# Performance work log

Measured on AMD Instinct MI355X. Metric: run time of the kernel, lower is better.

The kernel has to match this reference:

```python
import jax, jax.numpy as jnp
import numpy as np

B, S, D, H = 4, 2048, 1024, 16
HD = D // H  # head dim = 64


def setup_inputs() -> dict:
    key = jax.random.key(0)
    ks = jax.random.split(key, 11)
    s = 1.0 / np.sqrt(D)
    return {
        "xq": jax.random.normal(ks[0], (B, S, D), jnp.float32),
        "xk": jax.random.normal(ks[1], (B, S, D), jnp.float32),
        "xv": jax.random.normal(ks[2], (B, S, D), jnp.float32),
        "wq": jax.random.normal(ks[3], (D, D), jnp.float32) * s,
        "bq": jnp.zeros((D,), jnp.float32),
        "wk": jax.random.normal(ks[4], (D, D), jnp.float32) * s,
        "bk": jnp.zeros((D,), jnp.float32),
        "wv": jax.random.normal(ks[5], (D, D), jnp.float32) * s,
        "bv": jnp.zeros((D,), jnp.float32),
        "wo": jax.random.normal(ks[6], (D, D), jnp.float32) * s,
        "bo": jnp.zeros((D,), jnp.float32),
    }


def reference(xq, xk, xv, wq, bq, wk, bk, wv, bv, wo, bo):
    # linear projections (torch Linear: x @ W.T + b; weights here stored as [in, out])
    q = xq @ wq + bq  # [B,S,D]
    k = xk @ wk + bk
    v = xv @ wv + bv
    # split heads -> [B,H,S,HD]
    q = q.reshape(B, S, H, HD).transpose(0, 2, 1, 3)
    k = k.reshape(B, S, H, HD).transpose(0, 2, 1, 3)
    v = v.reshape(B, S, H, HD).transpose(0, 2, 1, 3)
    # scaled dot-product attention; scale by sqrt(head_dim)
    scores = jnp.einsum('bhqd,bhkd->bhqk', q, k) / jnp.sqrt(jnp.float32(HD))
    attn = jax.nn.softmax(scores, axis=-1)  # [B,H,S,S]
    out = jnp.einsum('bhqk,bhkd->bhqd', attn, v)
    # merge heads -> [B,S,D]
    concat = out.transpose(0, 2, 1, 3).reshape(B, S, D)
    return concat @ wo + bo
```

## Files before the change

kernel.cpp:

```cpp
#include <hip/hip_runtime.h>
#include <hip/hip_bf16.h>

typedef unsigned short u16;
typedef short bf16x8 __attribute__((ext_vector_type(8)));
typedef float f32x4  __attribute__((ext_vector_type(4)));
typedef unsigned short u16x4 __attribute__((ext_vector_type(4)));

#define B_  4
#define S_  2048
#define D_  1024
#define H_  16
#define HD_ 64
#define M_  (B_ * S_)

__device__ __forceinline__ u16 f2bf(float f) {
    unsigned int u = __builtin_bit_cast(unsigned int, f);
    u += 0x7fffu + ((u >> 16) & 1u);
    return (u16)(u >> 16);
}
__device__ __forceinline__ void gload_lds16(const void* g, void* l) {
    __builtin_amdgcn_global_load_lds(
        (const __attribute__((address_space(1))) void*)g,
        (__attribute__((address_space(3))) void*)l, 16, 0, 0);
}
__device__ __forceinline__ unsigned int cvtpk_bf16(float a, float b) {
    unsigned int r;
    asm("v_cvt_pk_bf16_f32 %0, %1, %2" : "=v"(r) : "v"(a), "v"(b));
    return r;
}

__global__ __launch_bounds__(256) void k_transpose_w(
    const float* __restrict__ w0, const float* __restrict__ w1,
    const float* __restrict__ w2, const float* __restrict__ w3,
    u16* __restrict__ wtbase) {
    __shared__ float tile[32][33];
    const float* W = blockIdx.z == 0 ? w0 : blockIdx.z == 1 ? w1
                   : blockIdx.z == 2 ? w2 : w3;
    u16* Wt = wtbase + (size_t)blockIdx.z * (D_ * D_);
    const int tx = threadIdx.x, ty = threadIdx.y;
    const int bx = blockIdx.x * 32, by = blockIdx.y * 32;
#pragma unroll
    for (int i = 0; i < 4; ++i)
        tile[ty + 8 * i][tx] = W[(size_t)(by + ty + 8 * i) * D_ + bx + tx];
    __syncthreads();
#pragma unroll
    for (int i = 0; i < 4; ++i)
        Wt[(size_t)(bx + ty + 8 * i) * D_ + by + tx] = f2bf(tile[tx][ty + 8 * i]);
}

__global__ __launch_bounds__(256) void k_gemm_qkv(
    const float* __restrict__ xq, const float* __restrict__ xk,
    const float* __restrict__ xv, const u16* __restrict__ wtbase,
    const float* __restrict__ bq, const float* __restrict__ bk,
    const float* __restrict__ bv, u16* __restrict__ qkvout) {
    __shared__ __align__(16) u16 As[128 * 32];
    __shared__ __align__(16) u16 Bs[128 * 32];

    const int bid = (int)blockIdx.x;
    const int l2  = (bid & 7) * 192 + (bid >> 3);
    const int z   = l2 >> 9;
    const int t512 = l2 & 511;
    const int m0 = (t512 >> 3) * 128;
    const int n0 = (t512 & 7) * 128;

    const float* X    = z == 0 ? xq : z == 1 ? xk : xv;
    const u16*   Wt   = wtbase + (size_t)z * (D_ * D_);
    const float* bias = z == 0 ? bq : z == 1 ? bk : bv;
    u16* out = qkvout + (size_t)z * ((size_t)M_ * D_);

    const int t = threadIdx.x;
    const int w = t >> 6, lane = t & 63;
    const int wm = w >> 1, wn = w & 1;
    const int lr = lane & 15, kg = lane >> 4;

    const int r0 = t >> 2;
    const int r1 = 64 + r0;
    const int cq = ((t & 3) ^ ((r0 >> 1) & 3)) * 8;

    const int alq = t & 3;
    u16* as0 = &As[r0 * 32 + ((alq ^ ((r0 >> 1) & 3)) * 8)];
    u16* as1 = as0 + 64 * 32;

    const u16* aAddr[4];
    const u16* bAddr[4];
#pragma unroll
    for (int m = 0; m < 4; ++m) {
        const int row = wm * 64 + m * 16 + lr;
        aAddr[m] = &As[row * 32 + ((kg ^ ((row >> 1) & 3)) * 8)];
    }
#pragma unroll
    for (int n = 0; n < 4; ++n) {
        const int row = wn * 64 + n * 16 + lr;
        bAddr[n] = &Bs[row * 32 + ((kg ^ ((row >> 1) & 3)) * 8)];
    }

    f32x4 acc[4][4] = {};
    f32x4 ax[2][2];
    {
        const float* p0 = X + (size_t)(m0 + r0) * D_ + alq * 8;
        ax[0][0] = *(const f32x4*)p0;
        ax[0][1] = *(const f32x4*)(p0 + 4);
        const float* p1 = X + (size_t)(m0 + 64 + r0) * D_ + alq * 8;
        ax[1][0] = *(const f32x4*)p1;
        ax[1][1] = *(const f32x4*)(p1 + 4);
    }

    for (int kt = 0; kt < D_; kt += 32) {
        __syncthreads();
        {
            uint4 w0 = { cvtpk_bf16(ax[0][0][0], ax[0][0][1]),
                         cvtpk_bf16(ax[0][0][2], ax[0][0][3]),
                         cvtpk_bf16(ax[0][1][0], ax[0][1][1]),
                         cvtpk_bf16(ax[0][1][2], ax[0][1][3]) };
            *(uint4*)as0 = w0;
            uint4 w1 = { cvtpk_bf16(ax[1][0][0], ax[1][0][1]),
                         cvtpk_bf16(ax[1][0][2], ax[1][0][3]),
                         cvtpk_bf16(ax[1][1][0], ax[1][1][1]),
                         cvtpk_bf16(ax[1][1][2], ax[1][1][3]) };
            *(uint4*)as1 = w1;
        }
        gload_lds16(Wt + (size_t)(n0 + r0) * D_ + kt + cq, (char*)Bs + w * 1024);
        gload_lds16(Wt + (size_t)(n0 + r1) * D_ + kt + cq, (char*)Bs + 4096 + w * 1024);
        __syncthreads();

        if (kt + 32 < D_) {
            const float* p0 = X + (size_t)(m0 + r0) * D_ + kt + 32 + alq * 8;
            ax[0][0] = *(const f32x4*)p0;
            ax[0][1] = *(const f32x4*)(p0 + 4);
            const float* p1 = X + (size_t)(m0 + 64 + r0) * D_ + kt + 32 + alq * 8;
            ax[1][0] = *(const f32x4*)p1;
            ax[1][1] = *(const f32x4*)(p1 + 4);
        }

        bf16x8 a[4], bb[4];
#pragma unroll
        for (int m = 0; m < 4; ++m) a[m]  = *(const bf16x8*)aAddr[m];
#pragma unroll
        for (int n = 0; n < 4; ++n) bb[n] = *(const bf16x8*)bAddr[n];
#pragma unroll
        for (int m = 0; m < 4; ++m)
#pragma unroll
            for (int n = 0; n < 4; ++n)
                acc[m][n] = __builtin_amdgcn_mfma_f32_16x16x32_bf16(
                    a[m], bb[n], acc[m][n], 0, 0, 0);
    }

#pragma unroll
    for (int n = 0; n < 4; ++n) {
        const int c  = n0 + wn * 64 + n * 16 + lr;
        const float bv2 = bias[c];
#pragma unroll
        for (int m = 0; m < 4; ++m) {
            const int rb = m0 + wm * 64 + m * 16 + kg * 4;
#pragma unroll
            for (int j = 0; j < 4; ++j)
                out[(size_t)(rb + j) * D_ + c] = f2bf(acc[m][n][j] + bv2);
        }
    }
}

__global__ __launch_bounds__(256) void k_gemm_o(
    const u16* __restrict__ A, const u16* __restrict__ Wt,
    const float* __restrict__ bias, float* __restrict__ out) {
    __shared__ __align__(16) u16 As[128 * 32];
    __shared__ __align__(16) u16 Bs[128 * 32];

    const int cpx = gridDim.x >> 3;
    const int bid = (int)blockIdx.x;
    const int l   = (bid & 7) * cpx + (bid >> 3);
    const int m0 = (l >> 3) * 128;
    const int n0 = (l & 7) * 128;

    const int t = threadIdx.x;
    const int w = t >> 6, lane = t & 63;
    const int wm = w >> 1, wn = w & 1;
    const int lr = lane & 15, kg = lane >> 4;

    const int r0 = t >> 2;
    const int r1 = 64 + r0;
    const int cq = ((t & 3) ^ ((r0 >> 1) & 3)) * 8;

    const u16* aAddr[4];
    const u16* bAddr[4];
#pragma unroll
    for (int m = 0; m < 4; ++m) {
        const int row = wm * 64 + m * 16 + lr;
        aAddr[m] = &As[row * 32 + ((kg ^ ((row >> 1) & 3)) * 8)];
    }
#pragma unroll
    for (int n = 0; n < 4; ++n) {
        const int row = wn * 64 + n * 16 + lr;
        bAddr[n] = &Bs[row * 32 + ((kg ^ ((row >> 1) & 3)) * 8)];
    }

    f32x4 acc[4][4] = {};

    for (int kt = 0; kt < D_; kt += 32) {
        __syncthreads();
        gload_lds16(A  + (size_t)(m0 + r0) * D_ + kt + cq, (char*)As + w * 1024);
        gload_lds16(A  + (size_t)(m0 + r1) * D_ + kt + cq, (char*)As + 4096 + w * 1024);
        gload_lds16(Wt + (size_t)(n0 + r0) * D_ + kt + cq, (char*)Bs + w * 1024);
        gload_lds16(Wt + (size_t)(n0 + r1) * D_ + kt + cq, (char*)Bs + 4096 + w * 1024);
        __syncthreads();

        bf16x8 a[4], bb[4];
#pragma unroll
        for (int m = 0; m < 4; ++m) a[m]  = *(const bf16x8*)aAddr[m];
#pragma unroll
        for (int n = 0; n < 4; ++n) bb[n] = *(const bf16x8*)bAddr[n];
#pragma unroll
        for (int m = 0; m < 4; ++m)
#pragma unroll
            for (int n = 0; n < 4; ++n)
                acc[m][n] = __builtin_amdgcn_mfma_f32_16x16x32_bf16(
                    a[m], bb[n], acc[m][n], 0, 0, 0);
    }

#pragma unroll
    for (int n = 0; n < 4; ++n) {
        const int c  = n0 + wn * 64 + n * 16 + lr;
        const float bv2 = bias[c];
#pragma unroll
        for (int m = 0; m < 4; ++m) {
            const int rb = m0 + wm * 64 + m * 16 + kg * 4;
#pragma unroll
            for (int j = 0; j < 4; ++j)
                out[(size_t)(rb + j) * D_ + c] = acc[m][n][j] + bv2;
        }
    }
}

__global__ __launch_bounds__(256) void k_attn(
    const u16* __restrict__ Qg, const u16* __restrict__ Kg,
    const u16* __restrict__ Vg, u16* __restrict__ concat) {
    __shared__ u16 Ks[64][72];
    __shared__ u16 Vt[64][72];
    __shared__ u16 Ps[4][32][72];

    const int tid = threadIdx.x;
    const int qb = blockIdx.x, h = blockIdx.y, b = blockIdx.z;

    const int wq = tid >> 6, lane = tid & 63;
    const int lr = lane & 15, kg = lane >> 4;
    const size_t brow = (size_t)b * S_;
    const int col0 = h * HD_;
    const int q0 = qb * 128 + wq * 32;

    bf16x8 qa[2][2];
#pragma unroll
    for (int qf = 0; qf < 2; ++qf)
#pragma unroll
        for (int hh = 0; hh < 2; ++hh)
            qa[qf][hh] = *(const bf16x8*)(Qg + (brow + q0 + qf * 16 + lr) * D_ +
                                          col0 + hh * 32 + kg * 8);

    f32x4 oacc[2][4] = {};
    float l_part[8];
#pragma unroll
    for (int i = 0; i < 8; ++i) l_part[i] = 0.f;

    const int skr = tid >> 2, skc = (tid & 3) * 16;
    const int p5 = tid & 31;
    const int vlr = p5 & 15, vcb = (p5 >> 4) * 2;
    const int kA  = vcb * 16 + vlr;
    const int svd = (tid >> 5) * 8;
    const int vk0 = vlr * 4 + vcb;

    uint4 kr0, kr1, vr0, vr1;
    {
        const u16* kp = Kg + (brow + skr) * D_ + col0 + skc;
        kr0 = *(const uint4*)kp; kr1 = *(const uint4*)(kp + 8);
        const u16* vp = Vg + (brow + kA) * D_ + col0 + svd;
        vr0 = *(const uint4*)vp; vr1 = *(const uint4*)(vp + 16 * D_);
    }

    const int NT = S_ / 64;
    for (int kt = 0; kt < NT; ++kt) {
        __syncthreads();
        {
            *(uint4*)&Ks[skr][skc]     = kr0;
            *(uint4*)&Ks[skr][skc + 8] = kr1;
            u16 va[8], vb8[8];
            *(uint4*)&va[0] = vr0;  *(uint4*)&vb8[0] = vr1;
#pragma unroll
            for (int i = 0; i < 8; ++i)
                *(unsigned int*)&Vt[svd + i][vk0] =
                    (unsigned int)va[i] | ((unsigned int)vb8[i] << 16);
        }
        __syncthreads();

        if (kt + 1 < NT) {
            const u16* kp = Kg + (brow + (kt + 1) * 64 + skr) * D_ + col0 + skc;
            kr0 = *(const uint4*)kp; kr1 = *(const uint4*)(kp + 8);
            const u16* vp = Vg + (brow + (kt + 1) * 64 + kA) * D_ + col0 + svd;
            vr0 = *(const uint4*)vp; vr1 = *(const uint4*)(vp + 16 * D_);
        }

        f32x4 sc[2][4] = {};
#pragma unroll
        for (int cb = 0; cb < 4; ++cb) {
            bf16x8 kb0 = *(const bf16x8*)&Ks[cb * 16 + lr][kg * 8];
            bf16x8 kb1 = *(const bf16x8*)&Ks[cb * 16 + lr][32 + kg * 8];
#pragma unroll
            for (int qf = 0; qf < 2; ++qf) {
                sc[qf][cb] = __builtin_amdgcn_mfma_f32_16x16x32_bf16(
                    qa[qf][0], kb0, sc[qf][cb], 0, 0, 0);
                sc[qf][cb] = __builtin_amdgcn_mfma_f32_16x16x32_bf16(
                    qa[qf][1], kb1, sc[qf][cb], 0, 0, 0);
            }
        }

#pragma unroll
        for (int qf = 0; qf < 2; ++qf)
#pragma unroll
            for (int j = 0; j < 4; ++j) {
                const int prow = qf * 16 + 4 * kg + j;
                const float pv0 = __expf(fmaf(sc[qf][0][j], 0.125f, -8.0f));
                const float pv1 = __expf(fmaf(sc[qf][1][j], 0.125f, -8.0f));
                const float pv2 = __expf(fmaf(sc[qf][2][j], 0.125f, -8.0f));
                const float pv3 = __expf(fmaf(sc[qf][3][j], 0.125f, -8.0f));
                l_part[qf * 4 + j] += (pv0 + pv1) + (pv2 + pv3);
                uint2 pw = { cvtpk_bf16(pv0, pv1), cvtpk_bf16(pv2, pv3) };
                *(uint2*)&Ps[wq][prow][lr * 4] = pw;
            }

#pragma unroll
        for (int hh = 0; hh < 2; ++hh) {
            bf16x8 pa0 = *(const bf16x8*)&Ps[wq][lr][hh * 32 + kg * 8];
            bf16x8 pa1 = *(const bf16x8*)&Ps[wq][16 + lr][hh * 32 + kg * 8];
#pragma unroll
            for (int db = 0; db < 4; ++db) {
                bf16x8 vv = *(const bf16x8*)&Vt[db * 16 + lr][hh * 32 + kg * 8];
                oacc[0][db] = __builtin_amdgcn_mfma_f32_16x16x32_bf16(
                    pa0, vv, oacc[0][db], 0, 0, 0);
                oacc[1][db] = __builtin_amdgcn_mfma_f32_16x16x32_bf16(
                    pa1, vv, oacc[1][db], 0, 0, 0);
            }
        }
    }

    float linv[8];
#pragma unroll
    for (int st = 0; st < 8; ++st) {
        float l = l_part[st];
#pragma unroll
        for (int msk = 1; msk <= 8; msk <<= 1) l += __shfl_xor(l, msk, 64);
        linv[st] = 1.0f / l;
    }
#pragma unroll
    for (int qf = 0; qf < 2; ++qf)
#pragma unroll
        for (int db = 0; db < 4; ++db)
#pragma unroll
            for (int j = 0; j < 4; ++j)
                concat[(brow + q0 + qf * 16 + 4 * kg + j) * D_ +
                       col0 + db * 16 + lr] =
                    f2bf(oacc[qf][db][j] * linv[qf * 4 + j]);
}

extern "C" void kernel_launch(void* const* d_in, const int* in_sizes, int n_in,
                              void* d_out, int out_size, void* d_ws, size_t ws_size,
                              hipStream_t stream) {
    const float* xq = (const float*)d_in[0];
    const float* xk = (const float*)d_in[1];
    const float* xv = (const float*)d_in[2];
    const float* wq = (const float*)d_in[3];
    const float* bq = (const float*)d_in[4];
    const float* wk = (const float*)d_in[5];
    const float* bk = (const float*)d_in[6];
    const float* wv = (const float*)d_in[7];
    const float* bv = (const float*)d_in[8];
    const float* wo = (const float*)d_in[9];
    const float* bo = (const float*)d_in[10];

    char* ws = (char*)d_ws;
    u16* wt  = (u16*)ws;
    u16* qkv = (u16*)(ws + (8ull << 20));
    u16* cc  = (u16*)(ws + (56ull << 20));

    k_transpose_w<<<dim3(32, 32, 4), dim3(32, 8), 0, stream>>>(wq, wk, wv, wo, wt);
    k_gemm_qkv<<<1536, 256, 0, stream>>>(xq, xk, xv, wt, bq, bk, bv, qkv);
    k_attn<<<dim3(16, 16, 4), 256, 0, stream>>>(
        qkv, qkv + (size_t)M_ * D_, qkv + 2ull * M_ * D_, cc);
    k_gemm_o<<<512, 256, 0, stream>>>(cc, wt + 3ull * D_ * D_, bo, (float*)d_out);
}
```

Baseline: 223.1 us.

## Double-buffer LDS tiles to prefetch next K-slice in QKV and output GEMMs

The weight tile in the QKV projection GEMM and both operand tiles in the output projection GEMM now use two LDS buffers. The next K-slice is issued via global_load_lds into the alternate buffer before the MFMAs on the current one, so the global-to-LDS traffic can overlap with compute. The output GEMM also drops one barrier per iteration. The cost is double the LDS for those tiles, which may reduce occupancy, and correctness depends on the barrier's implicit wait for the async LDS loads.

```diff
diff --git a/kernel.cpp b/kernel.cpp
--- a/kernel.cpp
+++ b/kernel.cpp
@@ -54,7 +54,7 @@
     const float* __restrict__ bq, const float* __restrict__ bk,
     const float* __restrict__ bv, u16* __restrict__ qkvout) {
     __shared__ __align__(16) u16 As[128 * 32];
-    __shared__ __align__(16) u16 Bs[128 * 32];
+    __shared__ __align__(16) u16 Bs[2][128 * 32];
 
     const int bid = (int)blockIdx.x;
     const int l2  = (bid & 7) * 192 + (bid >> 3);
@@ -82,7 +82,7 @@
     u16* as1 = as0 + 64 * 32;
 
     const u16* aAddr[4];
-    const u16* bAddr[4];
+    int bOff[4];
 #pragma unroll
     for (int m = 0; m < 4; ++m) {
         const int row = wm * 64 + m * 16 + lr;
@@ -91,7 +91,7 @@
 #pragma unroll
     for (int n = 0; n < 4; ++n) {
         const int row = wn * 64 + n * 16 + lr;
-        bAddr[n] = &Bs[row * 32 + ((kg ^ ((row >> 1) & 3)) * 8)];
+        bOff[n] = row * 32 + ((kg ^ ((row >> 1) & 3)) * 8);
     }
 
     f32x4 acc[4][4] = {};
@@ -103,9 +103,12 @@
         const float* p1 = X + (size_t)(m0 + 64 + r0) * D_ + alq * 8;
         ax[1][0] = *(const f32x4*)p1;
         ax[1][1] = *(const f32x4*)(p1 + 4);
+        gload_lds16(Wt + (size_t)(n0 + r0) * D_ + cq, (char*)&Bs[0][0] + w * 1024);
+        gload_lds16(Wt + (size_t)(n0 + r1) * D_ + cq, (char*)&Bs[0][0] + 4096 + w * 1024);
     }
 
     for (int kt = 0; kt < D_; kt += 32) {
+        const int cur = (kt >> 5) & 1;
         __syncthreads();
         {
             uint4 w0 = { cvtpk_bf16(ax[0][0][0], ax[0][0][1]),
@@ -119,11 +122,13 @@
                          cvtpk_bf16(ax[1][1][2], ax[1][1][3]) };
             *(uint4*)as1 = w1;
         }
-        gload_lds16(Wt + (size_t)(n0 + r0) * D_ + kt + cq, (char*)Bs + w * 1024);
-        gload_lds16(Wt + (size_t)(n0 + r1) * D_ + kt + cq, (char*)Bs + 4096 + w * 1024);
         __syncthreads();
 
         if (kt + 32 < D_) {
+            gload_lds16(Wt + (size_t)(n0 + r0) * D_ + kt + 32 + cq,
+                        (char*)&Bs[cur ^ 1][0] + w * 1024);
+            gload_lds16(Wt + (size_t)(n0 + r1) * D_ + kt + 32 + cq,
+                        (char*)&Bs[cur ^ 1][0] + 4096 + w * 1024);
             const float* p0 = X + (size_t)(m0 + r0) * D_ + kt + 32 + alq * 8;
             ax[0][0] = *(const f32x4*)p0;
             ax[0][1] = *(const f32x4*)(p0 + 4);
@@ -136,7 +141,7 @@
 #pragma unroll
         for (int m = 0; m < 4; ++m) a[m]  = *(const bf16x8*)aAddr[m];
 #pragma unroll
-        for (int n = 0; n < 4; ++n) bb[n] = *(const bf16x8*)bAddr[n];
+        for (int n = 0; n < 4; ++n) bb[n] = *(const bf16x8*)&Bs[cur][bOff[n]];
 #pragma unroll
         for (int m = 0; m < 4; ++m)
 #pragma unroll
@@ -162,8 +167,8 @@
 __global__ __launch_bounds__(256) void k_gemm_o(
     const u16* __restrict__ A, const u16* __restrict__ Wt,
     const float* __restrict__ bias, float* __restrict__ out) {
-    __shared__ __align__(16) u16 As[128 * 32];
-    __shared__ __align__(16) u16 Bs[128 * 32];
+    __shared__ __align__(16) u16 As[2][128 * 32];
+    __shared__ __align__(16) u16 Bs[2][128 * 32];
 
     const int cpx = gridDim.x >> 3;
     const int bid = (int)blockIdx.x;
@@ -180,34 +185,45 @@
     const int r1 = 64 + r0;
     const int cq = ((t & 3) ^ ((r0 >> 1) & 3)) * 8;
 
-    const u16* aAddr[4];
-    const u16* bAddr[4];
+    int aOff[4], bOff[4];
 #pragma unroll
     for (int m = 0; m < 4; ++m) {
         const int row = wm * 64 + m * 16 + lr;
-        aAddr[m] = &As[row * 32 + ((kg ^ ((row >> 1) & 3)) * 8)];
+        aOff[m] = row * 32 + ((kg ^ ((row >> 1) & 3)) * 8);
     }
 #pragma unroll
     for (int n = 0; n < 4; ++n) {
         const int row = wn * 64 + n * 16 + lr;
-        bAddr[n] = &Bs[row * 32 + ((kg ^ ((row >> 1) & 3)) * 8)];
+        bOff[n] = row * 32 + ((kg ^ ((row >> 1) & 3)) * 8);
     }
 
     f32x4 acc[4][4] = {};
 
+    gload_lds16(A  + (size_t)(m0 + r0) * D_ + cq, (char*)&As[0][0] + w * 1024);
+    gload_lds16(A  + (size_t)(m0 + r1) * D_ + cq, (char*)&As[0][0] + 4096 + w * 1024);
+    gload_lds16(Wt + (size_t)(n0 + r0) * D_ + cq, (char*)&Bs[0][0] + w * 1024);
+    gload_lds16(Wt + (size_t)(n0 + r1) * D_ + cq, (char*)&Bs[0][0] + 4096 + w * 1024);
+
     for (int kt = 0; kt < D_; kt += 32) {
+        const int cur = (kt >> 5) & 1;
         __syncthreads();
-        gload_lds16(A  + (size_t)(m0 + r0) * D_ + kt + cq, (char*)As + w * 1024);
-        gload_lds16(A  + (size_t)(m0 + r1) * D_ + kt + cq, (char*)As + 4096 + w * 1024);
-        gload_lds16(Wt + (size_t)(n0 + r0) * D_ + kt + cq, (char*)Bs + w * 1024);
-        gload_lds16(Wt + (size_t)(n0 + r1) * D_ + kt + cq, (char*)Bs + 4096 + w * 1024);
-        __syncthreads();
+
+        if (kt + 32 < D_) {
+            gload_lds16(A  + (size_t)(m0 + r0) * D_ + kt + 32 + cq,
+                        (char*)&As[cur ^ 1][0] + w * 1024);
+            gload_lds16(A  + (size_t)(m0 + r1) * D_ + kt + 32 + cq,
+                        (char*)&As[cur ^ 1][0] + 4096 + w * 1024);
+            gload_lds16(Wt + (size_t)(n0 + r0) * D_ + kt + 32 + cq,
+                        (char*)&Bs[cur ^ 1][0] + w * 1024);
+            gload_lds16(Wt + (size_t)(n0 + r1) * D_ + kt + 32 + cq,
+                        (char*)&Bs[cur ^ 1][0] + 4096 + w * 1024);
+        }
 
         bf16x8 a[4], bb[4];
 #pragma unroll
-        for (int m = 0; m < 4; ++m) a[m]  = *(const bf16x8*)aAddr[m];
-#pragma unroll
-        for (int n = 0; n < 4; ++n) bb[n] = *(const bf16x8*)bAddr[n];
+        for (int m = 0; m < 4; ++m) a[m]  = *(const bf16x8*)&As[cur][aOff[m]];
+#pragma unroll
+        for (int n = 0; n < 4; ++n) bb[n] = *(const bf16x8*)&Bs[cur][bOff[n]];
 #pragma unroll
         for (int m = 0; m < 4; ++m)
 #pragma unroll
```

Result: slower. 229.8 us (+3.0%).
